# Optimization experiments

Measured on AMD Instinct MI355X. Metric: run time of the kernel, lower is better.

Reference implementation:

```python
import jax, jax.numpy as jnp
import numpy as np

L = 2        # num_layers
H = 512      # hidden_size
IN = 32      # input_size = output_size + 24
OUT = 8      # output_size
B = 512      # batch
S = 128      # encoder seq_len
F = 48       # future_len
TF = 24      # time-feature dim


def setup_inputs() -> dict:
    key = jax.random.key(0)
    ks = jax.random.split(key, 14)
    def rn(k, shape, s=0.05):
        return jax.random.normal(k, shape, dtype=jnp.float32) * s
    return {
        "x": rn(ks[0], (S, B, IN), 1.0),
        "future_time": rn(ks[1], (F - 1, B, TF), 1.0),
        "h0": rn(ks[2], (L, 1, H), 1.0),
        "c0": rn(ks[3], (L, 1, H), 1.0),
        # PyTorch nn.LSTM weights: gate order (i, f, g, o), rows of 4H
        "w_ih0": rn(ks[4], (4 * H, IN)),
        "w_hh0": rn(ks[5], (4 * H, H)),
        "b_ih0": rn(ks[6], (4 * H,)),
        "b_hh0": rn(ks[7], (4 * H,)),
        "w_ih1": rn(ks[8], (4 * H, H)),
        "w_hh1": rn(ks[9], (4 * H, H)),
        "b_ih1": rn(ks[10], (4 * H,)),
        "b_hh1": rn(ks[11], (4 * H,)),
        "fc_w": rn(ks[12], (OUT, H)),
        "fc_b": rn(ks[13], (OUT,)),
    }


def _cell(x, h, c, w_ih, w_hh, b):
    # PyTorch LSTMCell math, gate order i,f,g,o
    gates = x @ w_ih.T + h @ w_hh.T + b  # [B, 4H]
    i, f, g, o = jnp.split(gates, 4, axis=-1)
    c2 = jax.nn.sigmoid(f) * c + jax.nn.sigmoid(i) * jnp.tanh(g)
    h2 = jax.nn.sigmoid(o) * jnp.tanh(c2)
    return h2, c2


def reference(x, future_time, h0, c0,
              w_ih0, w_hh0, b_ih0, b_hh0,
              w_ih1, w_hh1, b_ih1, b_hh1,
              fc_w, fc_b):
    batch = x.shape[1]
    params = [(w_ih0, w_hh0, b_ih0 + b_hh0),
              (w_ih1, w_hh1, b_ih1 + b_hh1)]
    h_init = jnp.broadcast_to(h0, (L, batch, H))
    c_init = jnp.broadcast_to(c0, (L, batch, H))

    def multi_step(carry, x_t):
        hs, cs = carry
        new_h, new_c = [], []
        inp = x_t
        for l, (wi, wh, b) in enumerate(params):
            h2, c2 = _cell(inp, hs[l], cs[l], wi, wh, b)
            new_h.append(h2)
            new_c.append(c2)
            inp = h2
        return (jnp.stack(new_h), jnp.stack(new_c)), inp

    # encoder pass over the conditioning sequence
    (hs, cs), outs = jax.lax.scan(multi_step, (h_init, c_init), x)
    y0 = outs[-1] @ fc_w.T + fc_b  # [B, OUT], first prediction

    def dec_step(carry, t_feat):
        hs, cs, y = carry
        x_t = jnp.concatenate([y, t_feat], axis=-1)  # [B, OUT+TF] == [B, IN]
        (hs2, cs2), h_top = multi_step((hs, cs), x_t)
        y2 = h_top @ fc_w.T + fc_b
        return (hs2, cs2, y2), y2

    _, ys = jax.lax.scan(dec_step, (hs, cs, y0), future_time)
    return jnp.concatenate([y0[None], ys], axis=0)  # [future_len, B, OUT]
```

## Files before the change

### kernel.cpp

```cpp
#include <hip/hip_runtime.h>


typedef __attribute__((ext_vector_type(8))) short bf16x8;
typedef __attribute__((ext_vector_type(16))) float f32x16;

#define MFMA32(a, b, c) __builtin_amdgcn_mfma_f32_32x32x16_bf16((a), (b), (c), 0, 0, 0)
#define DEV static __device__ __forceinline__

constexpr int kSeq = 128;
constexpr int kT = 175;
constexpr int kRB = 65536;

constexpr size_t kWsHbuf = 0;
constexpr size_t kWsYacc = 2ull * 2 * 8 * kRB;
constexpr size_t kWsFlag = kWsYacc + 2ull * 512 * 8 * 4;
constexpr size_t kWsRc   = kWsFlag + 2ull * 8 * 32 * 64;
constexpr size_t kWsEnd  = kWsRc + 2ull * 8 * 64;
constexpr size_t kWsZeroBegin = kWsYacc;
constexpr size_t kWsZeroSize  = kWsEnd - kWsYacc;

DEV unsigned short f2bf(float f) {
  unsigned u = __float_as_uint(f);
  u += 0x7fffu + ((u >> 16) & 1u);
  return (unsigned short)(u >> 16);
}
DEV float bf2f(unsigned short s) { return __uint_as_float(((unsigned)s) << 16); }
DEV float sigf(float v) { return 1.0f / (1.0f + __expf(-v)); }
DEV float tanhf_(float v) { float e = __expf(2.0f * v); return 1.0f - 2.0f / (e + 1.0f); }
DEV f32x16 zero16() {
  f32x16 z;
#pragma unroll
  for (int i = 0; i < 16; ++i) z[i] = 0.0f;
  return z;
}
DEV bf16x8 pack8(const float* p) {
  float4 a = *(const float4*)p;
  float4 b = *(const float4*)(p + 4);
  bf16x8 r;
  r[0] = (short)f2bf(a.x); r[1] = (short)f2bf(a.y);
  r[2] = (short)f2bf(a.z); r[3] = (short)f2bf(a.w);
  r[4] = (short)f2bf(b.x); r[5] = (short)f2bf(b.y);
  r[6] = (short)f2bf(b.z); r[7] = (short)f2bf(b.w);
  return r;
}

DEV unsigned ald(const unsigned* p) {
  return __hip_atomic_load(p, __ATOMIC_RELAXED, __HIP_MEMORY_SCOPE_AGENT);
}
DEV void ast(unsigned* p, unsigned v) {
  __hip_atomic_store(p, v, __ATOMIC_RELAXED, __HIP_MEMORY_SCOPE_AGENT);
}
DEV unsigned long long ald64(const unsigned long long* p) {
  return __hip_atomic_load(p, __ATOMIC_RELAXED, __HIP_MEMORY_SCOPE_AGENT);
}
DEV void ast64(unsigned long long* p, unsigned long long v) {
  __hip_atomic_store(p, v, __ATOMIC_RELAXED, __HIP_MEMORY_SCOPE_AGENT);
}
DEV float aldf(const float* p) {
  return __hip_atomic_load(p, __ATOMIC_RELAXED, __HIP_MEMORY_SCOPE_AGENT);
}
DEV void astf(float* p, float v) {
  __hip_atomic_store(p, v, __ATOMIC_RELAXED, __HIP_MEMORY_SCOPE_AGENT);
}
DEV void relwait() {
  __atomic_signal_fence(__ATOMIC_SEQ_CST);
  __builtin_amdgcn_s_waitcnt(0);
  __atomic_signal_fence(__ATOMIC_SEQ_CST);
}
DEV bool pollw(const unsigned* slot, unsigned thr) {
  for (int it = 0; it < (1 << 22); ++it) {
    const unsigned v = ald(slot);
    if (__ballot(v < thr) == 0ull) {
      __atomic_signal_fence(__ATOMIC_ACQUIRE);
      return true;
    }
    __builtin_amdgcn_s_sleep(1);
  }
  return false;
}

#define PARTS_WRITE(accv, ms_, ns_)                                           \
  { const int gate_ = (ns_)*2 + gbit;                                         \
    _Pragma("unroll") for (int rg = 0; rg < 16; ++rg) {                       \
      const int r_ = (ms_)*32 + (rg & 3) + 4 * hi5 + 8 * (rg >> 2);           \
      partsB[((kw * 4 + gate_) * 64 + r_) * 17 + l15] = f2bf((accv)[rg]);     \
    } }

__global__ __launch_bounds__(256, 2) void lstm_persist(
    const float* __restrict__ x, const float* __restrict__ ft,
    const float* __restrict__ h0in, const float* __restrict__ c0in,
    const float* __restrict__ wih0, const float* __restrict__ whh0,
    const float* __restrict__ bih0, const float* __restrict__ bhh0,
    const float* __restrict__ wih1, const float* __restrict__ whh1,
    const float* __restrict__ bih1, const float* __restrict__ bhh1,
    const float* __restrict__ fcw, const float* __restrict__ fcb,
    float* __restrict__ out, char* __restrict__ ws) {
  __shared__ __attribute__((aligned(16))) unsigned short partsB[16 * 64 * 17];
  __shared__ __attribute__((aligned(16))) unsigned short xin[64 * 40];
  __shared__ __attribute__((aligned(16))) unsigned short hloc[64 * 24];
  __shared__ float biasl[4][16];
  __shared__ float fcwl[8][16];
  __shared__ unsigned bflag;

  const int bid = blockIdx.x;
  const int layer = bid >> 8;
  const int idx = bid & 255;
  const int bc = idx & 7;
  const int hc = idx >> 3;
  const int b0 = bc * 64;
  const int u0 = hc * 16;
  const int tid = threadIdx.x;
  const int kw = tid >> 6;
  const int lane = tid & 63;
  const int l31 = lane & 31, l15 = lane & 15, hi5 = lane >> 5, gbit = (lane >> 4) & 1;

  char* hbuf = ws + kWsHbuf;
  float* yacc = (float*)(ws + kWsYacc);
  unsigned* flg = (unsigned*)(ws + kWsFlag);
  unsigned* rc = (unsigned*)(ws + kWsRc);

  auto fslot = [&](int l, int b, int h) { return flg + (((l * 8) + b) * 32 + h) * 16; };
  auto region = [&](int p, int l, int b) -> char* {
    return hbuf + (size_t)(((p * 2) + l) * 8 + b) * kRB;
  };

  bool alive = true;

  bf16x8 wf[2][16];
#pragma unroll
  for (int ns = 0; ns < 2; ++ns) {
    const int gate = ns * 2 + gbit;
    const int wrow = gate * 512 + u0 + l15;
    if (layer) {
#pragma unroll
      for (int m = 0; m < 16; ++m) {
        const int jg = kw + 4 * m;
        const int k0 = jg * 16 + hi5 * 8;
        const float* p = (k0 < 512) ? (wih1 + wrow * 512 + k0)
                                    : (whh1 + wrow * 512 + (k0 - 512));
        wf[ns][m] = pack8(p);
      }
    } else {
#pragma unroll
      for (int m = 0; m < 8; ++m) {
        const int jg = kw + 4 * m;
        wf[ns][m] = pack8(whh0 + wrow * 512 + jg * 16 + hi5 * 8);
      }
      if (kw < 2) wf[ns][8] = pack8(wih0 + wrow * 32 + kw * 16 + hi5 * 8);
    }
  }

  if (tid < 64) {
    const int g = tid >> 4, h = tid & 15;
    const int row = g * 512 + u0 + h;
    biasl[g][h] = layer ? (bih1[row] + bhh1[row]) : (bih0[row] + bhh0[row]);
  }
  if (layer && tid >= 64 && tid < 192) {
    const int t2 = tid - 64;
    fcwl[t2 >> 4][t2 & 15] = fcw[(t2 >> 4) * 512 + u0 + (t2 & 15)];
  }

  const int own_h = tid & 15;
  const int own_r0 = (tid >> 4) * 4;
  float cst[4];
  {
    const float cv = c0in[layer * 512 + u0 + own_h];
    cst[0] = cst[1] = cst[2] = cst[3] = cv;
  }

  {
    char* dst = region(layer ? 0 : 1, layer, bc);
    if (tid < 128) {
      const int r = tid >> 1, half = tid & 1;
      union { unsigned short s[8]; unsigned long long u[2]; } v;
#pragma unroll
      for (int k2 = 0; k2 < 8; ++k2)
        v.s[k2] = f2bf(h0in[layer * 512 + u0 + half * 8 + k2]);
      unsigned long long* dp =
          (unsigned long long*)(dst + ((u0 >> 3) + half) * 1024 + r * 16);
      ast64(dp, v.u[0]); ast64(dp + 1, v.u[1]);
    }
    relwait();
    __syncthreads();
    if (tid == 0) ast(fslot(layer, bc, hc), 1u);
  }

  auto xin_store = [&](int r, int c4, float4 v) {
    const int gx = c4 >> 3, half = (c4 >> 2) & 1;
    uint2 pv;
    pv.x = (unsigned)f2bf(v.x) | ((unsigned)f2bf(v.y) << 16);
    pv.y = (unsigned)f2bf(v.z) | ((unsigned)f2bf(v.w) << 16);
    *(uint2*)&xin[r * 40 + ((gx ^ (r & 3)) << 3) + half * 4] = pv;
  };

  auto cell_update = [&]() {
#pragma unroll
    for (int i = 0; i < 4; ++i) {
      const int r = own_r0 + i;
      float ig = biasl[0][own_h], fg = biasl[1][own_h];
      float gg = biasl[2][own_h], og = biasl[3][own_h];
#pragma unroll
      for (int w2 = 0; w2 < 4; ++w2) {
        ig += bf2f(partsB[((w2 * 4 + 0) * 64 + r) * 17 + own_h]);
        fg += bf2f(partsB[((w2 * 4 + 1) * 64 + r) * 17 + own_h]);
        gg += bf2f(partsB[((w2 * 4 + 2) * 64 + r) * 17 + own_h]);
        og += bf2f(partsB[((w2 * 4 + 3) * 64 + r) * 17 + own_h]);
      }
      const float cv = sigf(fg) * cst[i] + sigf(ig) * tanhf_(gg);
      cst[i] = cv;
      hloc[r * 24 + own_h] = f2bf(sigf(og) * tanhf_(cv));
    }
  };

  auto h_publish = [&](char* dst) {
    if (tid < 128) {
      const int r = tid >> 1, half = tid & 1;
      union { uint4 q; unsigned long long u[2]; } v;
      v.q = *(const uint4*)&hloc[r * 24 + half * 8];
      unsigned long long* dp =
          (unsigned long long*)(dst + ((u0 >> 3) + half) * 1024 + r * 16);
      ast64(dp, v.u[0]); ast64(dp + 1, v.u[1]);
    }
  };

  if (layer == 0) {
    for (int t = 0; t < kT; ++t) {
      if (kw == 0 && alive) {
        const unsigned* slot = (lane < 32)
            ? fslot(0, bc, lane)
            : fslot(1, bc, lane - 32);
        const unsigned thr = (lane < 32)
            ? (unsigned)(t + 1)
            : (unsigned)((t < kSeq) ? t : t + 1);
        alive = pollw(slot, thr);
      }
      __syncthreads();

      if (t < kSeq) {
#pragma unroll
        for (int it = 0; it < 2; ++it) {
          const int u = tid + it * 256;
          const int r = u >> 3, c4 = (u & 7) * 4;
          xin_store(r, c4, *(const float4*)&x[(size_t)(t * 512 + b0 + r) * 32 + c4]);
        }
        __syncthreads();
      } else {
        const int q = (t - 1) & 1;
        if (tid < 128) {
          const int r = tid >> 1, o4 = (tid & 1) * 4;
          const float* yp = &yacc[(size_t)(q * 512 + b0 + r) * 8 + o4];
          float4 v;
          v.x = aldf(yp + 0); v.y = aldf(yp + 1);
          v.z = aldf(yp + 2); v.w = aldf(yp + 3);
          const float4 bb = *(const float4*)&fcb[o4];
          v.x += bb.x; v.y += bb.y; v.z += bb.z; v.w += bb.w;
          if (hc == 0)
            *(float4*)&out[(size_t)((t - kSeq) * 512 + b0 + r) * 8 + o4] = v;
          xin_store(r, o4, v);
        }
        for (int u = tid; u < 384; u += 256) {
          const int r = u / 6, m = u - r * 6;
          xin_store(r, 8 + m * 4,
                    *(const float4*)&ft[(size_t)((t - kSeq) * 512 + b0 + r) * 24 + m * 4]);
        }
        __syncthreads();
        if (tid == 0) {
          const unsigned old = __hip_atomic_fetch_add(rc + (q * 8 + bc) * 16, 1u,
                                                      __ATOMIC_RELAXED,
                                                      __HIP_MEMORY_SCOPE_AGENT);
          bflag = (old == 31u) ? 1u : 0u;
        }
        __syncthreads();
        if (bflag) {
          for (int u = tid; u < 512; u += 256)
            astf(&yacc[(size_t)q * 512 * 8 + (size_t)b0 * 8 + u], 0.0f);
          relwait();
          __syncthreads();
          if (tid == 0) ast(rc + (q * 8 + bc) * 16, 0u);
        }
      }

      f32x16 acc00 = zero16(), acc01 = zero16(), acc10 = zero16(), acc11 = zero16();
      const char* hb0 = region((t - 1) & 1, 0, bc);
      unsigned long long abuf[2][16];
#pragma unroll
      for (int i = 0; i < 4; ++i) {
        const size_t off = (size_t)((2 * (kw + 4 * i) + hi5) * 64 + l31) * 16;
        const unsigned long long* p = (const unsigned long long*)(hb0 + off);
        abuf[0][i * 4 + 0] = ald64(p);
        abuf[0][i * 4 + 1] = ald64(p + 1);
        const unsigned long long* q2 = (const unsigned long long*)(hb0 + off + 512);
        abuf[0][i * 4 + 2] = ald64(q2);
        abuf[0][i * 4 + 3] = ald64(q2 + 1);
      }
#pragma unroll
      for (int g = 0; g < 2; ++g) {
        if (g == 0) {
#pragma unroll
          for (int i = 0; i < 4; ++i) {
            const int m = 4 + i;
            const size_t off = (size_t)((2 * (kw + 4 * m) + hi5) * 64 + l31) * 16;
            const unsigned long long* p = (const unsigned long long*)(hb0 + off);
            abuf[1][i * 4 + 0] = ald64(p);
            abuf[1][i * 4 + 1] = ald64(p + 1);
            const unsigned long long* q2 = (const unsigned long long*)(hb0 + off + 512);
            abuf[1][i * 4 + 2] = ald64(q2);
            abuf[1][i * 4 + 3] = ald64(q2 + 1);
          }
        }
#pragma unroll
        for (int i = 0; i < 4; ++i) {
          const int m = g * 4 + i;
          union { unsigned long long u[2]; bf16x8 v; } a0, a1;
          a0.u[0] = abuf[g][i * 4 + 0]; a0.u[1] = abuf[g][i * 4 + 1];
          a1.u[0] = abuf[g][i * 4 + 2]; a1.u[1] = abuf[g][i * 4 + 3];
          acc00 = MFMA32(a0.v, wf[0][m], acc00);
          acc01 = MFMA32(a0.v, wf[1][m], acc01);
          acc10 = MFMA32(a1.v, wf[0][m], acc10);
          acc11 = MFMA32(a1.v, wf[1][m], acc11);
        }
      }
      if (kw < 2) {
#pragma unroll
        for (int ms = 0; ms < 2; ++ms) {
          const int r = ms * 32 + l31;
          const int gx = kw * 2 + hi5;
          const bf16x8 a = *(const bf16x8*)&xin[r * 40 + ((gx ^ (r & 3)) << 3)];
          if (ms == 0) {
            acc00 = MFMA32(a, wf[0][8], acc00);
            acc01 = MFMA32(a, wf[1][8], acc01);
          } else {
            acc10 = MFMA32(a, wf[0][8], acc10);
            acc11 = MFMA32(a, wf[1][8], acc11);
          }
        }
      }
      PARTS_WRITE(acc00, 0, 0); PARTS_WRITE(acc01, 0, 1);
      PARTS_WRITE(acc10, 1, 0); PARTS_WRITE(acc11, 1, 1);
      __syncthreads();
      cell_update();
      __syncthreads();
      h_publish(region(t & 1, 0, bc));
      relwait();
      __syncthreads();
      if (tid == 0) ast(fslot(0, bc, hc), (unsigned)(t + 2));
    }
    if (hc == 0) {
      if (kw == 0 && alive)
        alive = pollw(fslot(1, bc, lane & 31), (unsigned)(kT + 1));
      __syncthreads();
      for (int u = tid; u < 512; u += 256) {
        const int r = u >> 3, o = u & 7;
        out[(size_t)(47 * 512 + b0 + r) * 8 + o] =
            aldf(&yacc[(size_t)(b0 + r) * 8 + o]) + fcb[o];
      }
    }
  } else {
    for (int t = 0; t < kT; ++t) {
      if (kw == 0 && alive) {
        const unsigned* slot = (lane < 32)
            ? fslot(0, bc, lane)
            : fslot(1, bc, lane - 32);
        const unsigned thr = (lane < 32) ? (unsigned)(t + 2) : (unsigned)(t + 1);
        alive = pollw(slot, thr);
      }
      __syncthreads();

      f32x16 acc00 = zero16(), acc01 = zero16(), acc10 = zero16(), acc11 = zero16();
      const char* hbA = region(t & 1, 0, bc);
      const char* hbB = region(t & 1, 1, bc);
      unsigned long long abuf[2][16];
#pragma unroll
      for (int i = 0; i < 4; ++i) {
        const char* base = hbA;
        const size_t off = (size_t)((2 * (kw + 4 * i) + hi5) * 64 + l31) * 16;
        const unsigned long long* p = (const unsigned long long*)(base + off);
        abuf[0][i * 4 + 0] = ald64(p);
        abuf[0][i * 4 + 1] = ald64(p + 1);
        const unsigned long long* q2 = (const unsigned long long*)(base + off + 512);
        abuf[0][i * 4 + 2] = ald64(q2);
        abuf[0][i * 4 + 3] = ald64(q2 + 1);
      }
#pragma unroll
      for (int g = 0; g < 4; ++g) {
        if (g < 3) {
          const int gn = g + 1;
#pragma unroll
          for (int i = 0; i < 4; ++i) {
            const int m = gn * 4 + i;
            const char* base = (m < 8) ? hbA : hbB;
            const int jl = (kw + 4 * m) & 31;
            const size_t off = (size_t)((2 * jl + hi5) * 64 + l31) * 16;
            const unsigned long long* p = (const unsigned long long*)(base + off);
            abuf[gn & 1][i * 4 + 0] = ald64(p);
            abuf[gn & 1][i * 4 + 1] = ald64(p + 1);
            const unsigned long long* q2 = (const unsigned long long*)(base + off + 512);
            abuf[gn & 1][i * 4 + 2] = ald64(q2);
            abuf[gn & 1][i * 4 + 3] = ald64(q2 + 1);
          }
        }
#pragma unroll
        for (int i = 0; i < 4; ++i) {
          const int m = g * 4 + i;
          union { unsigned long long u[2]; bf16x8 v; } a0, a1;
          a0.u[0] = abuf[g & 1][i * 4 + 0]; a0.u[1] = abuf[g & 1][i * 4 + 1];
          a1.u[0] = abuf[g & 1][i * 4 + 2]; a1.u[1] = abuf[g & 1][i * 4 + 3];
          acc00 = MFMA32(a0.v, wf[0][m], acc00);
          acc01 = MFMA32(a0.v, wf[1][m], acc01);
          acc10 = MFMA32(a1.v, wf[0][m], acc10);
          acc11 = MFMA32(a1.v, wf[1][m], acc11);
        }
      }
      PARTS_WRITE(acc00, 0, 0); PARTS_WRITE(acc01, 0, 1);
      PARTS_WRITE(acc10, 1, 0); PARTS_WRITE(acc11, 1, 1);
      __syncthreads();
      cell_update();
      __syncthreads();
      h_publish(region((t & 1) ^ 1, 1, bc));
      if (t >= kSeq - 1) {
        const int q = t & 1;
#pragma unroll
        for (int rep = 0; rep < 2; ++rep) {
          const int i2 = tid + rep * 256;
          const int r = i2 >> 3, o = i2 & 7;
          float s = 0.0f;
#pragma unroll
          for (int h2 = 0; h2 < 16; ++h2)
            s += bf2f(hloc[r * 24 + h2]) * fcwl[o][h2];
          atomicAdd(&yacc[(size_t)(q * 512 + b0 + r) * 8 + o], s);
        }
      }
      relwait();
      __syncthreads();
      if (tid == 0) ast(fslot(1, bc, hc), (unsigned)(t + 2));
    }
  }
}

extern "C" void kernel_launch(void* const* d_in, const int* in_sizes, int n_in,
                              void* d_out, int out_size, void* d_ws, size_t ws_size,
                              hipStream_t stream) {
  (void)in_sizes; (void)n_in; (void)out_size; (void)ws_size;
  hipMemsetAsync((char*)d_ws + kWsZeroBegin, 0, kWsZeroSize, stream);

  const float* x    = (const float*)d_in[0];
  const float* ft   = (const float*)d_in[1];
  const float* h0in = (const float*)d_in[2];
  const float* c0in = (const float*)d_in[3];
  const float* wih0 = (const float*)d_in[4];
  const float* whh0 = (const float*)d_in[5];
  const float* bih0 = (const float*)d_in[6];
  const float* bhh0 = (const float*)d_in[7];
  const float* wih1 = (const float*)d_in[8];
  const float* whh1 = (const float*)d_in[9];
  const float* bih1 = (const float*)d_in[10];
  const float* bhh1 = (const float*)d_in[11];
  const float* fcw  = (const float*)d_in[12];
  const float* fcb  = (const float*)d_in[13];
  float* out = (float*)d_out;
  char* ws = (char*)d_ws;

  void* args[] = {&x, &ft, &h0in, &c0in, &wih0, &whh0, &bih0, &bhh0,
                  &wih1, &whh1, &bih1, &bhh1, &fcw, &fcb, &out, &ws};
  hipError_t err = hipLaunchCooperativeKernel((void*)lstm_persist, dim3(512),
                                              dim3(256), args, 0, stream);
  if (err != hipSuccess) {
    lstm_persist<<<dim3(512), dim3(256), 0, stream>>>(
        x, ft, h0in, c0in, wih0, whh0, bih0, bhh0,
        wih1, whh1, bih1, bhh1, fcw, fcb, out, ws);
  }
}
```

Before: 3.361 ms.

## Replace per-block flag slots with shared atomic arrival counters

Per-block flag stores are replaced with one atomic fetch-add counter per (layer, batch chunk), so a poll reads two counters instead of 64 separate flag slots. In layer 0's encoder steps, the x load now happens before the wait, overlapping it with synchronization. The cost is that all 32 blocks contend on a single atomic address, and sleep between polls is longer, which may add wake-up latency.

Result: slower. 3.732 ms (+11.0%).

```diff
diff --git a/kernel.cpp b/kernel.cpp
--- a/kernel.cpp
+++ b/kernel.cpp
@@ -13,8 +13,8 @@
 
 constexpr size_t kWsHbuf = 0;
 constexpr size_t kWsYacc = 2ull * 2 * 8 * kRB;
-constexpr size_t kWsFlag = kWsYacc + 2ull * 512 * 8 * 4;
-constexpr size_t kWsRc   = kWsFlag + 2ull * 8 * 32 * 64;
+constexpr size_t kWsCnt  = kWsYacc + 2ull * 512 * 8 * 4;
+constexpr size_t kWsRc   = kWsCnt + 2ull * 8 * 128;
 constexpr size_t kWsEnd  = kWsRc + 2ull * 8 * 64;
 constexpr size_t kWsZeroBegin = kWsYacc;
 constexpr size_t kWsZeroSize  = kWsEnd - kWsYacc;
@@ -47,9 +47,6 @@
 DEV unsigned ald(const unsigned* p) {
   return __hip_atomic_load(p, __ATOMIC_RELAXED, __HIP_MEMORY_SCOPE_AGENT);
 }
-DEV void ast(unsigned* p, unsigned v) {
-  __hip_atomic_store(p, v, __ATOMIC_RELAXED, __HIP_MEMORY_SCOPE_AGENT);
-}
 DEV unsigned long long ald64(const unsigned long long* p) {
   return __hip_atomic_load(p, __ATOMIC_RELAXED, __HIP_MEMORY_SCOPE_AGENT);
 }
@@ -61,20 +58,26 @@
 }
 DEV void astf(float* p, float v) {
   __hip_atomic_store(p, v, __ATOMIC_RELAXED, __HIP_MEMORY_SCOPE_AGENT);
+}
+DEV void aadd(unsigned* p) {
+  __hip_atomic_fetch_add(p, 1u, __ATOMIC_RELAXED, __HIP_MEMORY_SCOPE_AGENT);
 }
 DEV void relwait() {
   __atomic_signal_fence(__ATOMIC_SEQ_CST);
   __builtin_amdgcn_s_waitcnt(0);
   __atomic_signal_fence(__ATOMIC_SEQ_CST);
 }
-DEV bool pollw(const unsigned* slot, unsigned thr) {
+DEV bool pollc(const unsigned* c0, unsigned t0, const unsigned* c1, unsigned t1) {
+  const int ln = (int)(threadIdx.x & 63);
+  const unsigned* p = (ln == 1) ? c1 : c0;
+  const unsigned thr = (ln == 0) ? t0 : ((ln == 1) ? t1 : 0u);
   for (int it = 0; it < (1 << 22); ++it) {
-    const unsigned v = ald(slot);
+    const unsigned v = (ln < 2) ? ald(p) : 0xffffffffu;
     if (__ballot(v < thr) == 0ull) {
       __atomic_signal_fence(__ATOMIC_ACQUIRE);
       return true;
     }
-    __builtin_amdgcn_s_sleep(1);
+    __builtin_amdgcn_s_sleep(2);
   }
   return false;
 }
@@ -116,10 +119,11 @@
 
   char* hbuf = ws + kWsHbuf;
   float* yacc = (float*)(ws + kWsYacc);
-  unsigned* flg = (unsigned*)(ws + kWsFlag);
+  unsigned* cntbase = (unsigned*)(ws + kWsCnt);
   unsigned* rc = (unsigned*)(ws + kWsRc);
 
-  auto fslot = [&](int l, int b, int h) { return flg + (((l * 8) + b) * 32 + h) * 16; };
+  unsigned* cs0 = cntbase + (0 * 8 + bc) * 32;
+  unsigned* cs1 = cntbase + (1 * 8 + bc) * 32;
   auto region = [&](int p, int l, int b) -> char* {
     return hbuf + (size_t)(((p * 2) + l) * 8 + b) * kRB;
   };
@@ -182,7 +186,7 @@
     }
     relwait();
     __syncthreads();
-    if (tid == 0) ast(fslot(layer, bc, hc), 1u);
+    if (tid == 0) aadd(layer ? cs1 : cs0);
   }
 
   auto xin_store = [&](int r, int c4, float4 v) {
@@ -225,17 +229,7 @@
 
   if (layer == 0) {
     for (int t = 0; t < kT; ++t) {
-      if (kw == 0 && alive) {
-        const unsigned* slot = (lane < 32)
-            ? fslot(0, bc, lane)
-            : fslot(1, bc, lane - 32);
-        const unsigned thr = (lane < 32)
-            ? (unsigned)(t + 1)
-            : (unsigned)((t < kSeq) ? t : t + 1);
-        alive = pollw(slot, thr);
-      }
-      __syncthreads();
-
+      const unsigned c0thr = 32u * (unsigned)(t + 1);
       if (t < kSeq) {
 #pragma unroll
         for (int it = 0; it < 2; ++it) {
@@ -243,8 +237,13 @@
           const int r = u >> 3, c4 = (u & 7) * 4;
           xin_store(r, c4, *(const float4*)&x[(size_t)(t * 512 + b0 + r) * 32 + c4]);
         }
+        if (kw == 0 && alive)
+          alive = pollc(cs0, c0thr, cs1, 32u * (unsigned)t);
         __syncthreads();
       } else {
+        if (kw == 0 && alive)
+          alive = pollc(cs0, c0thr, cs1, 32u * (unsigned)(t + 1));
+        __syncthreads();
         const int q = (t - 1) & 1;
         if (tid < 128) {
           const int r = tid >> 1, o4 = (tid & 1) * 4;
@@ -276,7 +275,9 @@
             astf(&yacc[(size_t)q * 512 * 8 + (size_t)b0 * 8 + u], 0.0f);
           relwait();
           __syncthreads();
-          if (tid == 0) ast(rc + (q * 8 + bc) * 16, 0u);
+          if (tid == 0)
+            __hip_atomic_store(rc + (q * 8 + bc) * 16, 0u, __ATOMIC_RELAXED,
+                               __HIP_MEMORY_SCOPE_AGENT);
         }
       }
 
@@ -343,11 +344,11 @@
       h_publish(region(t & 1, 0, bc));
       relwait();
       __syncthreads();
-      if (tid == 0) ast(fslot(0, bc, hc), (unsigned)(t + 2));
+      if (tid == 0) aadd(cs0);
     }
     if (hc == 0) {
       if (kw == 0 && alive)
-        alive = pollw(fslot(1, bc, lane & 31), (unsigned)(kT + 1));
+        alive = pollc(cs1, 32u * (unsigned)(kT + 1), cs1, 0u);
       __syncthreads();
       for (int u = tid; u < 512; u += 256) {
         const int r = u >> 3, o = u & 7;
@@ -357,13 +358,8 @@
     }
   } else {
     for (int t = 0; t < kT; ++t) {
-      if (kw == 0 && alive) {
-        const unsigned* slot = (lane < 32)
-            ? fslot(0, bc, lane)
-            : fslot(1, bc, lane - 32);
-        const unsigned thr = (lane < 32) ? (unsigned)(t + 2) : (unsigned)(t + 1);
-        alive = pollw(slot, thr);
-      }
+      if (kw == 0 && alive)
+        alive = pollc(cs0, 32u * (unsigned)(t + 2), cs1, 32u * (unsigned)(t + 1));
       __syncthreads();
 
       f32x16 acc00 = zero16(), acc01 = zero16(), acc10 = zero16(), acc11 = zero16();
@@ -432,7 +428,7 @@
       }
       relwait();
       __syncthreads();
-      if (tid == 0) ast(fslot(1, bc, hc), (unsigned)(t + 2));
+      if (tid == 0) aadd(cs1);
     }
   }
 }
```
